# Optimization experiments

Hardware: AMD Instinct MI355X
Metric: run time of the kernel (lower is better)

Reference implementation:

```python
import jax, jax.numpy as jnp
import numpy as np

NUM_EXPERTS = 8
TOP_K = 2


def setup_inputs() -> dict:
    key = jax.random.key(0)
    ks = jax.random.split(key, 5)
    B, N, E, H, X = 8, 2048, 512, 768, NUM_EXPERTS
    s_in = 0.02
    return {
        "x": jax.random.normal(ks[0], (B, N, E), dtype=jnp.float32),
        "Wg": jax.random.normal(ks[1], (E, X), dtype=jnp.float32) * s_in,
        "bg": jnp.zeros((X,), dtype=jnp.float32),
        "W1": jax.random.normal(ks[2], (X, E, H), dtype=jnp.float32) * (1.0 / np.sqrt(E)),
        "b1": jnp.zeros((X, H), dtype=jnp.float32),
        "W2": jax.random.normal(ks[3], (X, H, E), dtype=jnp.float32) * (1.0 / np.sqrt(H)),
        "b2": jnp.zeros((X, E), dtype=jnp.float32),
    }


def reference(x, Wg, bg, W1, b1, W2, b2):
    # Router: scores over experts, top-k, softmax over the k selected logits
    scores = jnp.einsum("bne,ex->bnx", x, Wg) + bg            # [B,N,X]
    topk_vals, topk_idx = jax.lax.top_k(scores, TOP_K)         # [B,N,K]
    gates = jax.nn.softmax(topk_vals, axis=-1)                 # [B,N,K]

    # Dense per-expert MLP (GELU exact, matching torch nn.GELU default)
    h = jnp.einsum("bne,xeh->bnxh", x, W1) + b1                # [B,N,X,H]
    h = jax.nn.gelu(h, approximate=False)
    expert_out = jnp.einsum("bnxh,xhe->bnxe", h, W2) + b2      # [B,N,X,E]

    # Combine: out = sum_k gate_k * expert_{idx_k}(x)
    onehot = jax.nn.one_hot(topk_idx, NUM_EXPERTS, dtype=x.dtype)  # [B,N,K,X]
    combine = jnp.einsum("bnk,bnkx->bnx", gates, onehot)           # [B,N,X]
    out = jnp.einsum("bnx,bnxe->bne", combine, expert_out)         # [B,N,E]
    return out
```

## Files before the change

kernel.cpp:

```cpp
#include <hip/hip_runtime.h>
#include <math.h>
#include <stdint.h>

typedef unsigned short u16;
typedef unsigned int u32;
typedef __attribute__((ext_vector_type(8))) short bf16x8;
typedef __attribute__((ext_vector_type(4))) float f32x4;

#define T_TOK 16384
#define NEXP 8
#define HROWS 33792
#define ROWT 264

__device__ __forceinline__ u16 f2bf(float f) {
    union { float f; unsigned u; } v; v.f = f;
    unsigned u = v.u;
    return (u16)((u + 0x7fffu + ((u >> 16) & 1u)) >> 16);
}

__device__ __forceinline__ float gelu_exact(float h) {
    float x  = h * 0.70710678118654752f;
    float ax = fabsf(x);
    float t  = __builtin_amdgcn_rcpf(1.f + 0.3275911f * ax);
    float p  = t * (0.254829592f + t * (-0.284496736f + t * (1.421413741f +
               t * (-1.453152027f + t * 1.061405429f))));
    float er = 1.f - p * __expf(-x * x);
    er = (x < 0.f) ? -er : er;
    return 0.5f * h * (1.f + er);
}

__device__ __forceinline__ void gload16(const void* g, void* l) {
    __builtin_amdgcn_global_load_lds(
        (const __attribute__((address_space(1))) u32*)(unsigned long long)(uintptr_t)g,
        (__attribute__((address_space(3))) u32*)(unsigned int)(uintptr_t)l,
        16, 0, 0);
}

__device__ __forceinline__ double shfl_xor_dbl(double v, int m) {
    union { double d; int i[2]; } u; u.d = v;
    u.i[0] = __shfl_xor(u.i[0], m, 64);
    u.i[1] = __shfl_xor(u.i[1], m, 64);
    return u.d;
}

__global__ void transpose_all_kernel(const float* __restrict__ W1, const float* __restrict__ W2,
                                     u16* __restrict__ W1t, u16* __restrict__ W2t) {
    __shared__ float tile[32][33];
    int id = blockIdx.x;
    const float* src; u16* dst; int R, C, e, c0, r0;
    if (id < 3072) {
        R = 512; C = 768; e = id / 384; int rem = id % 384;
        c0 = (rem % 24) * 32; r0 = (rem / 24) * 32;
        src = W1; dst = W1t;
    } else {
        id -= 3072;
        R = 768; C = 512; e = id / 384; int rem = id % 384;
        c0 = (rem % 16) * 32; r0 = (rem / 16) * 32;
        src = W2; dst = W2t;
    }
    int tx = threadIdx.x & 31, ty = threadIdx.x >> 5;
    const float* s = src + (size_t)e * R * C;
#pragma unroll
    for (int i = 0; i < 32; i += 8)
        tile[ty + i][tx] = s[(size_t)(r0 + ty + i) * C + (c0 + tx)];
    __syncthreads();
    u16* d = dst + (size_t)e * R * C;
#pragma unroll
    for (int i = 0; i < 32; i += 8)
        d[(size_t)(c0 + ty + i) * R + (r0 + tx)] = f2bf(tile[tx][ty + i]);
}

__global__ __launch_bounds__(256) void router_kernel(
    const float* __restrict__ x, const float* __restrict__ Wg,
    const float* __restrict__ bg,
    u16* __restrict__ xb, float4* __restrict__ packed, int* __restrict__ blockcnt) {
    __shared__ double wgd[4096];
    __shared__ int lcnt[8];
    int tid = threadIdx.x;
    if (tid < 8) lcnt[tid] = 0;
    for (int i = tid; i < 4096; i += 256) {
        int k = i >> 3, j = i & 7;
        int slot = (j + ((k >> 2) & 7)) & 7;
        wgd[k * 8 + slot] = (double)Wg[i];
    }
    __syncthreads();

    int w = tid >> 6, lane = tid & 63;
    int tg = lane >> 3, sl = lane & 7;
    int t  = blockIdx.x * 32 + w * 8 + tg;
    const float* xr = x  + (size_t)t * 512;
    u16*       xrow = xb + (size_t)t * 512;

    float4 xv[16];
#pragma unroll
    for (int it = 0; it < 16; it++)
        xv[it] = *(const float4*)(xr + it * 32 + sl * 4);

#pragma unroll
    for (int it = 0; it < 16; it++) {
        ushort4 o;
        o.x = f2bf(xv[it].x); o.y = f2bf(xv[it].y);
        o.z = f2bf(xv[it].z); o.w = f2bf(xv[it].w);
        *(ushort4*)(xrow + it * 32 + sl * 4) = o;
    }

    int jr[8];
#pragma unroll
    for (int j = 0; j < 8; j++) jr[j] = (j + sl) & 7;

    double acc[8];
#pragma unroll
    for (int j = 0; j < 8; j++) acc[j] = 0.0;
#pragma unroll
    for (int it = 0; it < 16; it++) {
        float vv[4] = { xv[it].x, xv[it].y, xv[it].z, xv[it].w };
#pragma unroll
        for (int q = 0; q < 4; q++) {
            int k = it * 32 + sl * 4 + q;
            double dv = (double)vv[q];
            const double* wr = wgd + (size_t)k * 8;
#pragma unroll
            for (int j = 0; j < 8; j++)
                acc[j] += dv * wr[jr[j]];
        }
    }
#pragma unroll
    for (int j = 0; j < 8; j++) {
        acc[j] += shfl_xor_dbl(acc[j], 1);
        acc[j] += shfl_xor_dbl(acc[j], 2);
        acc[j] += shfl_xor_dbl(acc[j], 4);
    }

    double s[8];
#pragma unroll
    for (int j = 0; j < 8; j++) s[j] = acc[j] + (double)bg[j];
    int i0 = 0;
#pragma unroll
    for (int j = 1; j < 8; j++) if (s[j] > s[i0]) i0 = j;
    int i1 = (i0 == 0) ? 1 : 0;
#pragma unroll
    for (int j = 0; j < 8; j++) if (j != i0 && s[j] > s[i1]) i1 = j;
    float d  = expf((float)(s[i1] - s[i0]));
    float g0 = 1.f / (1.f + d);
    float g1 = d / (1.f + d);

    if (sl == 0) {
        packed[t] = make_float4(__int_as_float(i0), __int_as_float(i1), g0, g1);
        atomicAdd(&lcnt[i0], 1);
        atomicAdd(&lcnt[i1], 1);
    }
    __syncthreads();
    if (tid < 8) blockcnt[blockIdx.x * 8 + tid] = lcnt[tid];
}

__global__ __launch_bounds__(512) void scan_kernel(const int* __restrict__ blockcnt,
                                                   int* __restrict__ blockoff,
                                                   int* __restrict__ counts) {
    int w = threadIdx.x >> 6;
    int lane = threadIdx.x & 63;
    int v[8]; int partial = 0;
#pragma unroll
    for (int i = 0; i < 8; i++) { v[i] = blockcnt[(lane * 8 + i) * 8 + w]; partial += v[i]; }
    int inc = partial;
#pragma unroll
    for (int d = 1; d < 64; d <<= 1) {
        int tt = __shfl_up(inc, d, 64);
        if (lane >= d) inc += tt;
    }
    int run = inc - partial;
#pragma unroll
    for (int i = 0; i < 8; i++) { blockoff[(lane * 8 + i) * 8 + w] = run; run += v[i]; }
    if (lane == 63) counts[w] = inc;
}

__global__ void scatter_kernel(const float4* __restrict__ packed,
                               const int* __restrict__ blockoff,
                               int* __restrict__ tokenlist, float* __restrict__ gatelist) {
    int b = blockIdx.x, i = threadIdx.x;
    int t = b * 32 + (i >> 1), p = i & 1;
    float4 pk = packed[t];
    int   e = p ? __float_as_int(pk.y) : __float_as_int(pk.x);
    float g = p ? pk.w : pk.z;
    unsigned long long lt = (1ull << i) - 1ull;
    int slot = 0;
#pragma unroll
    for (int j = 0; j < 8; j++) {
        unsigned long long m = __ballot(e == j);
        if (e == j) slot = blockoff[b * 8 + j] + __popcll(m & lt);
    }
    tokenlist[e * T_TOK + slot] = t;
    gatelist [e * T_TOK + slot] = g;
}

template<int PASS>
__global__ __launch_bounds__(256) void moe_gemm(
    const u16* __restrict__ A, const u16* __restrict__ W,
    const float* __restrict__ bias,
    const int* __restrict__ counts,
    const int* __restrict__ tokenlist, const float* __restrict__ gatelist,
    u16* __restrict__ Hout, float* __restrict__ out)
{
    constexpr int N = (PASS == 1) ? 768 : 512;
    constexpr int K = (PASS == 1) ? 512 : 768;

    __shared__ __align__(16) char smem[32768];
    __shared__ int   tokrow[128];
    __shared__ float gaterow[128];
    __shared__ int   spo[9];

    int tid = threadIdx.x;
    int rt  = blockIdx.x % ROWT;
    int ct  = blockIdx.x / ROWT;
    int row0 = rt * 128;

    if (tid == 0) {
        int s = 0;
#pragma unroll
        for (int e = 0; e < NEXP; e++) { spo[e] = s; s += (counts[e] + 127) & ~127; }
        spo[NEXP] = s;
    }
    __syncthreads();
    if (row0 >= spo[8]) return;
    int e = 0;
    while (row0 >= spo[e + 1]) e++;
    int lr0 = row0 - spo[e];
    int cnt = counts[e];
    if (tid < 128) {
        int slot = lr0 + tid;
        int cl   = slot < cnt ? slot : cnt - 1;
        tokrow[tid]  = tokenlist[e * T_TOK + cl];
        gaterow[tid] = gatelist[e * T_TOK + cl];
    }
    __syncthreads();

    int n0 = ct * 128;
    char* As = smem;
    char* Bs = smem + 16384;

    const u16* aptr[4];
    const u16* bptr[4];
    const u16* wbase = W + (size_t)e * ((size_t)N * K);
#pragma unroll
    for (int iss = 0; iss < 4; iss++) {
        int chunk = iss * 256 + tid;
        int row   = chunk >> 3;
        int c16   = (chunk & 7) ^ (row & 7);
        if (PASS == 1)
            aptr[iss] = A + (size_t)tokrow[row] * K + c16 * 8;
        else
            aptr[iss] = A + (size_t)(row0 + row) * K + c16 * 8;
        bptr[iss] = wbase + (size_t)(n0 + row) * K + c16 * 8;
    }

    int lane = tid & 63, w = tid >> 6;
    int wr = w >> 1, wc = w & 1;
    int lr = lane & 15, hk = lane >> 4;

    f32x4 acc[4][4];
#pragma unroll
    for (int mi = 0; mi < 4; mi++)
#pragma unroll
        for (int ni = 0; ni < 4; ni++)
            acc[mi][ni] = (f32x4){0.f, 0.f, 0.f, 0.f};

    for (int kk = 0; kk < K; kk += 64) {
#pragma unroll
        for (int iss = 0; iss < 4; iss++) {
            gload16(aptr[iss] + kk, As + (iss * 256 + tid) * 16);
            gload16(bptr[iss] + kk, Bs + (iss * 256 + tid) * 16);
        }
        __syncthreads();
#pragma unroll
        for (int ks = 0; ks < 2; ks++) {
            bf16x8 af[4], bfr[4];
#pragma unroll
            for (int mi = 0; mi < 4; mi++) {
                int row = wr * 64 + mi * 16 + lr;
                af[mi] = *(const bf16x8*)(As + row * 128 + (((ks * 4 + hk) ^ (row & 7)) * 16));
            }
#pragma unroll
            for (int ni = 0; ni < 4; ni++) {
                int row = wc * 64 + ni * 16 + lr;
                bfr[ni] = *(const bf16x8*)(Bs + row * 128 + (((ks * 4 + hk) ^ (row & 7)) * 16));
            }
#pragma unroll
            for (int mi = 0; mi < 4; mi++)
#pragma unroll
                for (int ni = 0; ni < 4; ni++)
                    acc[mi][ni] = __builtin_amdgcn_mfma_f32_16x16x32_bf16(
                        af[mi], bfr[ni], acc[mi][ni], 0, 0, 0);
        }
        __syncthreads();
    }

    if (PASS == 1) {
#pragma unroll
        for (int ni = 0; ni < 4; ni++) {
            int lcol = wc * 64 + ni * 16 + lr;
            float bb = bias[e * N + n0 + lcol];
#pragma unroll
            for (int mi = 0; mi < 4; mi++) {
#pragma unroll
                for (int r = 0; r < 4; r++) {
                    int row = wr * 64 + mi * 16 + hk * 4 + r;
                    *(u16*)(smem + row * 256 + lcol * 2) = f2bf(gelu_exact(acc[mi][ni][r] + bb));
                }
            }
        }
        __syncthreads();
#pragma unroll
        for (int iss = 0; iss < 8; iss++) {
            int chunk = iss * 256 + tid;
            int row = chunk >> 4, c16 = chunk & 15;
            uint4 v = *(const uint4*)(smem + row * 256 + c16 * 16);
            *(uint4*)(Hout + (size_t)(row0 + row) * 768 + n0 + c16 * 8) = v;
        }
    } else {
#pragma unroll
        for (int ni = 0; ni < 4; ni++) {
            int gcol = n0 + wc * 64 + ni * 16 + lr;
            float bb = bias[e * N + gcol];
#pragma unroll
            for (int mi = 0; mi < 4; mi++) {
#pragma unroll
                for (int r = 0; r < 4; r++) {
                    int row  = wr * 64 + mi * 16 + hk * 4 + r;
                    int slot = lr0 + row;
                    if (slot < cnt) {
                        int   tok = tokrow[row];
                        float g   = gaterow[row];
                        atomicAdd(out + (size_t)tok * 512 + gcol,
                                  (acc[mi][ni][r] + bb) * g);
                    }
                }
            }
        }
    }
}

extern "C" void kernel_launch(void* const* d_in, const int* in_sizes, int n_in,
                              void* d_out, int out_size, void* d_ws, size_t ws_size,
                              hipStream_t stream) {
    const float* x  = (const float*)d_in[0];
    const float* Wg = (const float*)d_in[1];
    const float* bg = (const float*)d_in[2];
    const float* W1 = (const float*)d_in[3];
    const float* b1 = (const float*)d_in[4];
    const float* W2 = (const float*)d_in[5];
    const float* b2 = (const float*)d_in[6];
    float* out = (float*)d_out;

    char* ws = (char*)d_ws;
    int*    counts    = (int*)(ws + 0);
    int*    blockcnt  = (int*)(ws + 1024);
    int*    blockoff  = (int*)(ws + 17408);
    float4* packed    = (float4*)(ws + 33792);
    int*    tokenlist = (int*)(ws + 295936);
    float*  gatelist  = (float*)(ws + 820224);
    u16*    xb        = (u16*)(ws + 1344512);
    u16*    W1t       = (u16*)(ws + 18121728);
    u16*    W2t       = (u16*)(ws + 24413184);
    u16*    H         = (u16*)(ws + 30704640);
    (void)in_sizes; (void)n_in; (void)ws_size;

    hipMemsetAsync(d_out, 0, (size_t)out_size * sizeof(float), stream);

    router_kernel<<<512, 256, 0, stream>>>(x, Wg, bg, xb, packed, blockcnt);
    transpose_all_kernel<<<6144, 256, 0, stream>>>(W1, W2, W1t, W2t);
    scan_kernel<<<1, 512, 0, stream>>>(blockcnt, blockoff, counts);
    scatter_kernel<<<512, 64, 0, stream>>>(packed, blockoff, tokenlist, gatelist);

    moe_gemm<1><<<6 * ROWT, 256, 0, stream>>>(xb, W1t, b1, counts,
                                              tokenlist, gatelist, H, nullptr);
    moe_gemm<2><<<4 * ROWT, 256, 0, stream>>>(H, W2t, b2, counts,
                                              tokenlist, gatelist, nullptr, out);
}
```

Before: 307.2 us.

## Fuse both expert GEMMs into one kernel with pre-fragmented weights

Replaces the two-pass grouped GEMM, which wrote the intermediate H activations to global memory, with one kernel per 64-token expert tile. The tile computes X·W1, applies bias and GELU into a 96KB LDS buffer, then multiplies by W2 and atomically accumulates into the output. The weight-prep kernel now lays W1/W2 out in MFMA fragment order so the GEMM loop reads B operands straight from global memory without LDS staging. This removes the H round trip and a launch, but needs about 129KB of LDS per block and reads weight fragments from global/L2 with no software pipelining.

```diff
diff --git a/kernel.cpp b/kernel.cpp
--- a/kernel.cpp
+++ b/kernel.cpp
@@ -9,8 +9,6 @@
 
 #define T_TOK 16384
 #define NEXP 8
-#define HROWS 33792
-#define ROWT 264
 
 __device__ __forceinline__ u16 f2bf(float f) {
     union { float f; unsigned u; } v; v.f = f;
@@ -43,31 +41,39 @@
     return u.d;
 }
 
-__global__ void transpose_all_kernel(const float* __restrict__ W1, const float* __restrict__ W2,
-                                     u16* __restrict__ W1t, u16* __restrict__ W2t) {
-    __shared__ float tile[32][33];
+__global__ __launch_bounds__(256) void wfrag_kernel(
+    const float* __restrict__ W1, const float* __restrict__ W2,
+    u16* __restrict__ W1f, u16* __restrict__ W2f) {
+    __shared__ float tile[32][65];
     int id = blockIdx.x;
-    const float* src; u16* dst; int R, C, e, c0, r0;
-    if (id < 3072) {
-        R = 512; C = 768; e = id / 384; int rem = id % 384;
-        c0 = (rem % 24) * 32; r0 = (rem / 24) * 32;
-        src = W1; dst = W1t;
+    const float* src; u16* dst; int K, N, e, k0, n0;
+    if (id < 1536) {
+        K = 512; N = 768; e = id / 192; int rem = id % 192;
+        k0 = (rem / 12) * 32; n0 = (rem % 12) * 64;
+        src = W1; dst = W1f;
     } else {
-        id -= 3072;
-        R = 768; C = 512; e = id / 384; int rem = id % 384;
-        c0 = (rem % 16) * 32; r0 = (rem / 16) * 32;
-        src = W2; dst = W2t;
-    }
-    int tx = threadIdx.x & 31, ty = threadIdx.x >> 5;
-    const float* s = src + (size_t)e * R * C;
-#pragma unroll
-    for (int i = 0; i < 32; i += 8)
-        tile[ty + i][tx] = s[(size_t)(r0 + ty + i) * C + (c0 + tx)];
-    __syncthreads();
-    u16* d = dst + (size_t)e * R * C;
-#pragma unroll
-    for (int i = 0; i < 32; i += 8)
-        d[(size_t)(c0 + ty + i) * R + (r0 + tx)] = f2bf(tile[tx][ty + i]);
+        id -= 1536;
+        K = 768; N = 512; e = id / 192; int rem = id % 192;
+        k0 = (rem / 8) * 32; n0 = (rem % 8) * 64;
+        src = W2; dst = W2f;
+    }
+    int tid = threadIdx.x;
+    const float* s = src + (size_t)e * K * N + (size_t)k0 * N + n0;
+#pragma unroll
+    for (int it = 0; it < 8; it++) {
+        int idx = it * 256 + tid;
+        int kk = idx >> 6, nn = idx & 63;
+        tile[kk][nn] = s[(size_t)kk * N + nn];
+    }
+    __syncthreads();
+    int w = tid >> 6, lane = tid & 63;
+    int c = w * 16 + (lane & 15), ksub = (lane >> 4) * 8;
+    union { u16 a[8]; uint4 v; } o;
+#pragma unroll
+    for (int j = 0; j < 8; j++) o.a[j] = f2bf(tile[ksub + j][c]);
+    int KF = K >> 5;
+    int nf = (n0 >> 4) + w, kf = k0 >> 5;
+    *(uint4*)(dst + (size_t)e * 393216 + ((size_t)(nf * KF + kf) * 64 + lane) * 8) = o.v;
 }
 
 __global__ __launch_bounds__(256) void router_kernel(
@@ -192,147 +198,154 @@
     gatelist [e * T_TOK + slot] = g;
 }
 
-template<int PASS>
-__global__ __launch_bounds__(256) void moe_gemm(
-    const u16* __restrict__ A, const u16* __restrict__ W,
-    const float* __restrict__ bias,
-    const int* __restrict__ counts,
-    const int* __restrict__ tokenlist, const float* __restrict__ gatelist,
-    u16* __restrict__ Hout, float* __restrict__ out)
+__global__ __launch_bounds__(512, 2) void fused_expert_kernel(
+    const u16* __restrict__ xb, const u16* __restrict__ W1f, const u16* __restrict__ W2f,
+    const float* __restrict__ b1, const float* __restrict__ b2,
+    const int* __restrict__ counts, const int* __restrict__ tokenlist,
+    const float* __restrict__ gatelist, float* __restrict__ out)
 {
-    constexpr int N = (PASS == 1) ? 768 : 512;
-    constexpr int K = (PASS == 1) ? 512 : 768;
-
-    __shared__ __align__(16) char smem[32768];
-    __shared__ int   tokrow[128];
-    __shared__ float gaterow[128];
-    __shared__ int   spo[9];
+    int e = blockIdx.x & 7;
+    int g = blockIdx.x >> 3;
+    int cnt = counts[e];
+    int row0 = g * 64;
+    if (row0 >= cnt) return;
+
+    __shared__ __align__(16) char smem[131840];
+    char* Xl = smem;
+    char* Hl = smem + 32768;
+    int*   tokrow  = (int*)(smem + 131072);
+    float* gaterow = (float*)(smem + 131328);
 
     int tid = threadIdx.x;
-    int rt  = blockIdx.x % ROWT;
-    int ct  = blockIdx.x / ROWT;
-    int row0 = rt * 128;
-
-    if (tid == 0) {
-        int s = 0;
-#pragma unroll
-        for (int e = 0; e < NEXP; e++) { spo[e] = s; s += (counts[e] + 127) & ~127; }
-        spo[NEXP] = s;
-    }
-    __syncthreads();
-    if (row0 >= spo[8]) return;
-    int e = 0;
-    while (row0 >= spo[e + 1]) e++;
-    int lr0 = row0 - spo[e];
-    int cnt = counts[e];
-    if (tid < 128) {
-        int slot = lr0 + tid;
-        int cl   = slot < cnt ? slot : cnt - 1;
+    if (tid < 64) {
+        int slot = row0 + tid;
+        int cl = slot < cnt ? slot : cnt - 1;
         tokrow[tid]  = tokenlist[e * T_TOK + cl];
         gaterow[tid] = gatelist[e * T_TOK + cl];
     }
     __syncthreads();
 
-    int n0 = ct * 128;
-    char* As = smem;
-    char* Bs = smem + 16384;
+    int lane = tid & 63, w = tid >> 6;
+    int lr = lane & 15, hk = lane >> 4;
 
     const u16* aptr[4];
-    const u16* bptr[4];
-    const u16* wbase = W + (size_t)e * ((size_t)N * K);
-#pragma unroll
-    for (int iss = 0; iss < 4; iss++) {
-        int chunk = iss * 256 + tid;
-        int row   = chunk >> 3;
-        int c16   = (chunk & 7) ^ (row & 7);
-        if (PASS == 1)
-            aptr[iss] = A + (size_t)tokrow[row] * K + c16 * 8;
-        else
-            aptr[iss] = A + (size_t)(row0 + row) * K + c16 * 8;
-        bptr[iss] = wbase + (size_t)(n0 + row) * K + c16 * 8;
-    }
-
-    int lane = tid & 63, w = tid >> 6;
-    int wr = w >> 1, wc = w & 1;
-    int lr = lane & 15, hk = lane >> 4;
-
-    f32x4 acc[4][4];
+#pragma unroll
+    for (int i = 0; i < 4; i++) {
+        int chunk = i * 512 + tid;
+        int row = chunk >> 5, c = chunk & 31;
+        int csrc = (c & 24) | ((c & 7) ^ (row & 7));
+        aptr[i] = xb + (size_t)tokrow[row] * 512 + csrc * 8;
+    }
+
+    const u16* w1b = W1f + (size_t)e * 393216;
+    const u16* w2b = W2f + (size_t)e * 393216;
+
+    f32x4 acc1[4][6];
 #pragma unroll
     for (int mi = 0; mi < 4; mi++)
 #pragma unroll
+        for (int ni = 0; ni < 6; ni++)
+            acc1[mi][ni] = (f32x4){0.f, 0.f, 0.f, 0.f};
+
+#pragma unroll
+    for (int h = 0; h < 2; h++) {
+        if (h) __syncthreads();
+#pragma unroll
+        for (int i = 0; i < 4; i++)
+            gload16(aptr[i] + h * 256, Xl + (i * 512 + tid) * 16);
+        __syncthreads();
+#pragma unroll
+        for (int ks = 0; ks < 8; ks++) {
+            bf16x8 a[4], b[6];
+#pragma unroll
+            for (int mi = 0; mi < 4; mi++) {
+                int row = mi * 16 + lr;
+                int chunk = ks * 4 + hk;
+                int sw = (chunk & 24) | ((chunk & 7) ^ (row & 7));
+                a[mi] = *(const bf16x8*)(Xl + row * 512 + sw * 16);
+            }
+            int kf = h * 8 + ks;
+#pragma unroll
+            for (int ni = 0; ni < 6; ni++) {
+                int nf = w * 6 + ni;
+                b[ni] = *(const bf16x8*)(w1b + ((nf * 16 + kf) * 64 + lane) * 8);
+            }
+#pragma unroll
+            for (int mi = 0; mi < 4; mi++)
+#pragma unroll
+                for (int ni = 0; ni < 6; ni++)
+                    acc1[mi][ni] = __builtin_amdgcn_mfma_f32_16x16x32_bf16(
+                        a[mi], b[ni], acc1[mi][ni], 0, 0, 0);
+        }
+    }
+
+    float b1v[6];
+#pragma unroll
+    for (int ni = 0; ni < 6; ni++) b1v[ni] = b1[e * 768 + w * 96 + ni * 16 + lr];
+#pragma unroll
+    for (int ni = 0; ni < 6; ni++) {
+        int col = w * 96 + ni * 16 + lr;
+        int cb = col >> 3;
+        int lo = (col * 2) & 15;
+#pragma unroll
+        for (int mi = 0; mi < 4; mi++) {
+#pragma unroll
+            for (int r = 0; r < 4; r++) {
+                int row = mi * 16 + hk * 4 + r;
+                int sw = (cb & ~7) | ((cb & 7) ^ (row & 7));
+                *(u16*)(Hl + row * 1536 + sw * 16 + lo) =
+                    f2bf(gelu_exact(acc1[mi][ni][r] + b1v[ni]));
+            }
+        }
+    }
+    __syncthreads();
+
+    f32x4 acc2[4][4];
+#pragma unroll
+    for (int mi = 0; mi < 4; mi++)
+#pragma unroll
         for (int ni = 0; ni < 4; ni++)
-            acc[mi][ni] = (f32x4){0.f, 0.f, 0.f, 0.f};
-
-    for (int kk = 0; kk < K; kk += 64) {
-#pragma unroll
-        for (int iss = 0; iss < 4; iss++) {
-            gload16(aptr[iss] + kk, As + (iss * 256 + tid) * 16);
-            gload16(bptr[iss] + kk, Bs + (iss * 256 + tid) * 16);
-        }
-        __syncthreads();
-#pragma unroll
-        for (int ks = 0; ks < 2; ks++) {
-            bf16x8 af[4], bfr[4];
-#pragma unroll
-            for (int mi = 0; mi < 4; mi++) {
-                int row = wr * 64 + mi * 16 + lr;
-                af[mi] = *(const bf16x8*)(As + row * 128 + (((ks * 4 + hk) ^ (row & 7)) * 16));
-            }
-#pragma unroll
-            for (int ni = 0; ni < 4; ni++) {
-                int row = wc * 64 + ni * 16 + lr;
-                bfr[ni] = *(const bf16x8*)(Bs + row * 128 + (((ks * 4 + hk) ^ (row & 7)) * 16));
-            }
-#pragma unroll
-            for (int mi = 0; mi < 4; mi++)
+            acc2[mi][ni] = (f32x4){0.f, 0.f, 0.f, 0.f};
+
+#pragma unroll
+    for (int ks = 0; ks < 24; ks++) {
+        bf16x8 a[4], b[4];
+#pragma unroll
+        for (int mi = 0; mi < 4; mi++) {
+            int row = mi * 16 + lr;
+            int chunk = ks * 4 + hk;
+            int sw = (chunk & ~7) | ((chunk & 7) ^ (row & 7));
+            a[mi] = *(const bf16x8*)(Hl + row * 1536 + sw * 16);
+        }
+#pragma unroll
+        for (int ni = 0; ni < 4; ni++) {
+            int nf = w * 4 + ni;
+            b[ni] = *(const bf16x8*)(w2b + ((nf * 24 + ks) * 64 + lane) * 8);
+        }
+#pragma unroll
+        for (int mi = 0; mi < 4; mi++)
+#pragma unroll
+            for (int ni = 0; ni < 4; ni++)
+                acc2[mi][ni] = __builtin_amdgcn_mfma_f32_16x16x32_bf16(
+                    a[mi], b[ni], acc2[mi][ni], 0, 0, 0);
+    }
+
+    float b2v[4];
+#pragma unroll
+    for (int ni = 0; ni < 4; ni++) b2v[ni] = b2[e * 512 + w * 64 + ni * 16 + lr];
+#pragma unroll
+    for (int mi = 0; mi < 4; mi++) {
+#pragma unroll
+        for (int r = 0; r < 4; r++) {
+            int row  = mi * 16 + hk * 4 + r;
+            int slot = row0 + row;
+            if (slot < cnt) {
+                int   tok = tokrow[row];
+                float gg  = gaterow[row];
+                float* orow = out + (size_t)tok * 512 + w * 64 + lr;
 #pragma unroll
                 for (int ni = 0; ni < 4; ni++)
-                    acc[mi][ni] = __builtin_amdgcn_mfma_f32_16x16x32_bf16(
-                        af[mi], bfr[ni], acc[mi][ni], 0, 0, 0);
-        }
-        __syncthreads();
-    }
-
-    if (PASS == 1) {
-#pragma unroll
-        for (int ni = 0; ni < 4; ni++) {
-            int lcol = wc * 64 + ni * 16 + lr;
-            float bb = bias[e * N + n0 + lcol];
-#pragma unroll
-            for (int mi = 0; mi < 4; mi++) {
-#pragma unroll
-                for (int r = 0; r < 4; r++) {
-                    int row = wr * 64 + mi * 16 + hk * 4 + r;
-                    *(u16*)(smem + row * 256 + lcol * 2) = f2bf(gelu_exact(acc[mi][ni][r] + bb));
-                }
-            }
-        }
-        __syncthreads();
-#pragma unroll
-        for (int iss = 0; iss < 8; iss++) {
-            int chunk = iss * 256 + tid;
-            int row = chunk >> 4, c16 = chunk & 15;
-            uint4 v = *(const uint4*)(smem + row * 256 + c16 * 16);
-            *(uint4*)(Hout + (size_t)(row0 + row) * 768 + n0 + c16 * 8) = v;
-        }
-    } else {
-#pragma unroll
-        for (int ni = 0; ni < 4; ni++) {
-            int gcol = n0 + wc * 64 + ni * 16 + lr;
-            float bb = bias[e * N + gcol];
-#pragma unroll
-            for (int mi = 0; mi < 4; mi++) {
-#pragma unroll
-                for (int r = 0; r < 4; r++) {
-                    int row  = wr * 64 + mi * 16 + hk * 4 + r;
-                    int slot = lr0 + row;
-                    if (slot < cnt) {
-                        int   tok = tokrow[row];
-                        float g   = gaterow[row];
-                        atomicAdd(out + (size_t)tok * 512 + gcol,
-                                  (acc[mi][ni][r] + bb) * g);
-                    }
-                }
+                    atomicAdd(orow + ni * 16, (acc2[mi][ni][r] + b2v[ni]) * gg);
             }
         }
     }
@@ -358,20 +371,17 @@
     int*    tokenlist = (int*)(ws + 295936);
     float*  gatelist  = (float*)(ws + 820224);
     u16*    xb        = (u16*)(ws + 1344512);
-    u16*    W1t       = (u16*)(ws + 18121728);
-    u16*    W2t       = (u16*)(ws + 24413184);
-    u16*    H         = (u16*)(ws + 30704640);
+    u16*    W1f       = (u16*)(ws + 18121728);
+    u16*    W2f       = (u16*)(ws + 24413184);
     (void)in_sizes; (void)n_in; (void)ws_size;
 
     hipMemsetAsync(d_out, 0, (size_t)out_size * sizeof(float), stream);
 
     router_kernel<<<512, 256, 0, stream>>>(x, Wg, bg, xb, packed, blockcnt);
-    transpose_all_kernel<<<6144, 256, 0, stream>>>(W1, W2, W1t, W2t);
+    wfrag_kernel<<<3072, 256, 0, stream>>>(W1, W2, W1f, W2f);
     scan_kernel<<<1, 512, 0, stream>>>(blockcnt, blockoff, counts);
     scatter_kernel<<<512, 64, 0, stream>>>(packed, blockoff, tokenlist, gatelist);
 
-    moe_gemm<1><<<6 * ROWT, 256, 0, stream>>>(xb, W1t, b1, counts,
-                                              tokenlist, gatelist, H, nullptr);
-    moe_gemm<2><<<4 * ROWT, 256, 0, stream>>>(H, W2t, b2, counts,
-                                              tokenlist, gatelist, nullptr, out);
-}
+    fused_expert_kernel<<<2048, 512, 0, stream>>>(xb, W1f, W2f, b1, b2,
+                                                  counts, tokenlist, gatelist, out);
+}
```

Measured after the change: 269.3 us. 1.14x faster.
